# Kernel optimization log

Hardware: AMD Instinct MI355X
Metric: run time of the kernel (lower is better)

Reference implementation:

```python
import jax, jax.numpy as jnp
import numpy as np
from jax import lax

N = 100000          # nodes in the AST
D = 128             # embedding_dims
C = 8               # max arity (complete 8-ary tree)
NTYPES = 131        # len(NODE_TYPES)


def setup_inputs() -> dict:
    key = jax.random.key(0)
    k_t, k_e, k_ih, k_hh = jax.random.split(key, 4)

    # --- build complete 8-ary tree structure (numpy, static) ---
    idx = np.arange(1, N)
    par = (idx - 1) // C
    slot = (idx - 1) % C
    children = np.full((N, C), N, dtype=np.int32)   # pad with sentinel N
    children[par, slot] = idx
    num_children = np.bincount(par, minlength=N).astype(np.int32)
    # depth of node i in complete C-ary tree: level d starts at (C^d-1)/(C-1)
    starts = np.array([(C ** d - 1) // (C - 1) for d in range(12)], dtype=np.int64)
    depth = np.searchsorted(starts, np.arange(N), side='right') - 1
    L = int(depth.max()) + 1
    M = int(np.bincount(depth).max())
    level_nodes = np.full((L, M), N, dtype=np.int32)  # deepest level first
    for d in range(L):
        nd = np.nonzero(depth == d)[0].astype(np.int32)
        level_nodes[L - 1 - d, : len(nd)] = nd

    # --- parameters (xavier-ish embedding, small LSTM weights, torch bias init) ---
    emb_table = jax.random.normal(k_e, (NTYPES, D), jnp.float32) * (2.0 / (NTYPES + D)) ** 0.5
    W_ih = jax.random.normal(k_ih, (4 * D, D), jnp.float32) * (2.0 / (5 * D)) ** 0.5
    W_hh = jax.random.normal(k_hh, (4 * D, D), jnp.float32) * (2.0 / (5 * D)) ** 0.5
    b_ih = jnp.zeros((4 * D,), jnp.float32)
    b_hh = jnp.ones((4 * D,), jnp.float32)
    node_types = jax.random.randint(k_t, (N,), 0, NTYPES, dtype=jnp.int32)
    return {
        'emb_table': emb_table, 'W_ih': W_ih, 'W_hh': W_hh,
        'b_ih': b_ih, 'b_hh': b_hh,
        'node_types': node_types,
        'children': jnp.asarray(children),
        'num_children': jnp.asarray(num_children),
        'level_nodes': jnp.asarray(level_nodes),
    }


def _forward(emb_table, W_ih, W_hh, b_ih, b_hh, node_types, children, num_children, level_nodes):
    M = level_nodes.shape[1]
    T = C + 1  # sequence length = parent emb + up to C child results

    def level_step(results, nodes):
        # nodes: [M] node ids for this depth level (sentinel N = padding)
        emb = emb_table[node_types[nodes]]            # [M, D] (OOB gather clips; masked below)
        nc = num_children[nodes]                      # [M]
        cres = results[children[nodes]]               # [M, C, D]; sentinel -> zero row N
        seq = jnp.concatenate([emb[:, None, :], cres], axis=1)  # [M, T, D]

        def cell(carry, xt):
            h, c = carry
            x, t = xt
            gates = x @ W_ih.T + b_ih + h @ W_hh.T + b_hh      # [M, 4D]
            i, f, g, o = jnp.split(gates, 4, axis=-1)
            i = jax.nn.sigmoid(i); f = jax.nn.sigmoid(f)
            g = jnp.tanh(g); o = jax.nn.sigmoid(o)
            c_new = f * c + i * g
            h_new = o * jnp.tanh(c_new)
            valid = (t <= nc)[:, None]                         # steps 0..nc are real
            return (jnp.where(valid, h_new, h), jnp.where(valid, c_new, c)), None

        h0 = jnp.zeros((M, emb_table.shape[1]), emb_table.dtype)
        (h, _), _ = lax.scan(cell, (h0, h0), (seq.transpose(1, 0, 2), jnp.arange(T)))
        out = jnp.where((nc == 0)[:, None], emb, h)   # leaves: raw embedding, no LSTM
        results = results.at[nodes].set(out)
        results = results.at[N].set(0.0)              # keep sentinel row zero
        return results, None

    results0 = jnp.zeros((N + 1, emb_table.shape[1]), emb_table.dtype)
    results, _ = lax.scan(level_step, results0, level_nodes)  # deepest -> root
    return results[0]  # root (Module node) encoding, shape [D]


def reference(emb_table, W_ih, W_hh, b_ih, b_hh, node_types, children, num_children, level_nodes):
    return _forward(emb_table, W_ih, W_hh, b_ih, b_hh,
                    node_types, children, num_children, level_nodes)
```

## Files before the change

### kernel.cpp

```cpp
#include <hip/hip_runtime.h>


#define D 128
#define NTOT 100000
#define NINT 12500

typedef _Float16 f16x8 __attribute__((ext_vector_type(8)));
typedef _Float16 f16x4 __attribute__((ext_vector_type(4)));
typedef float f32x4 __attribute__((ext_vector_type(4)));

__device__ __forceinline__ float fsig(float x) {
    float e = __expf(fminf(-x, 30.f));
    return __builtin_amdgcn_rcpf(1.f + e);
}
__device__ __forceinline__ float ftanh(float x) {
    float e = __expf(fminf(2.f * x, 30.f));
    return (e - 1.f) * __builtin_amdgcn_rcpf(e + 1.f);
}

__global__ void prep_wfrag(const float* __restrict__ W_ih, const float* __restrict__ W_hh,
                           const float* __restrict__ b_ih, const float* __restrict__ b_hh,
                           _Float16* __restrict__ wfrag, float4* __restrict__ bias4)
{
    int t = blockIdx.x * blockDim.x + threadIdx.x;
    if (t < 8 * 4 * 8 * 64) {
        int l  = t & 63;
        int kk = (t >> 6) & 7;
        int ct = (t >> 9) & 3;
        int w  = (t >> 11) & 7;
        int k0 = kk * 32 + ((l >> 4) * 8);
        int c  = ct * 128 + w * 16 + (l & 15);
        const float* src = (k0 < 128) ? (W_ih + (size_t)c * D + k0)
                                      : (W_hh + (size_t)c * D + (k0 - 128));
        f16x8 v;
#pragma unroll
        for (int j = 0; j < 8; ++j) v[j] = (_Float16)src[j];
        *(f16x8*)(wfrag + (size_t)t * 8) = v;
    }
    if (t < D) {
        bias4[t] = make_float4(b_ih[t      ] + b_hh[t      ],
                               b_ih[t + 128] + b_hh[t + 128],
                               b_ih[t + 256] + b_hh[t + 256],
                               b_ih[t + 384] + b_hh[t + 384]);
    }
}

template<int RT>
__global__ __launch_bounds__(512, 2) void lstm_level(
    int start, int count,
    const float* __restrict__ emb, const int* __restrict__ node_types,
    const int* __restrict__ children,
    const _Float16* __restrict__ wfrag, const float4* __restrict__ bias4,
    _Float16* __restrict__ resultsH, float* __restrict__ out)
{
    constexpr int NR  = 16 * RT;
    constexpr int TPR = 512 / NR;
    constexpr int DPT = 128 / TPR;

    __shared__ _Float16 Xh[NR][264];
    __shared__ int chid_s[NR][8];
    __shared__ int chty_s[NR][8];
    __shared__ int ntype_s[NR];

    const int t = threadIdx.x;
    const int w = t >> 6;
    const int l = t & 63;
    const int n0 = start + (int)blockIdx.x * NR;
    const int B  = min(NR, start + count - n0);

    f16x8 bf[4][8];
#pragma unroll
    for (int ct = 0; ct < 4; ++ct)
#pragma unroll
        for (int kk = 0; kk < 8; ++kk)
            bf[ct][kk] = *(const f16x8*)(wfrag + ((size_t)(((w * 4 + ct) * 8 + kk) * 64 + l)) * 8);

    const int dcol = w * 16 + (l & 15);
    const float4 bb = bias4[dcol];

    if (t < NR * 8) {
        int row = t >> 3, slot = t & 7;
        int ch = children[(size_t)(n0 + row) * 8 + slot];
        chid_s[row][slot] = ch;
        chty_s[row][slot] = (ch >= NINT && ch < NTOT) ? node_types[ch] : 0;
    }
    if (t < NR) ntype_s[t] = node_types[n0 + t];
    {
        int row = t / TPR, di = (t % TPR) * DPT;
        if (RT == 2) *(f16x8*)&Xh[row][128 + di] = (f16x8)(_Float16)0.f;
        else         *(f16x4*)&Xh[row][128 + di] = (f16x4)(_Float16)0.f;
    }

    float cr[RT][4], hr[RT][4];
#pragma unroll
    for (int rt = 0; rt < RT; ++rt)
#pragma unroll
        for (int r = 0; r < 4; ++r) { cr[rt][r] = 0.f; hr[rt][r] = 0.f; }

    __syncthreads();

    for (int s = 0; s < 9; ++s) {
        {
            const int row = t / TPR;
            const int di  = (t % TPR) * DPT;
            const float*     srcF = nullptr;
            const _Float16*  srcH = nullptr;
            if (s == 0) {
                srcF = emb + (size_t)ntype_s[row] * D;
            } else {
                int ch = chid_s[row][s - 1];
                if (ch < NINT)      srcH = resultsH + (size_t)ch * D;
                else if (ch < NTOT) srcF = emb + (size_t)chty_s[row][s - 1] * D;
            }
            if (RT == 2) {
                f16x8 v = (f16x8)(_Float16)0.f;
                if (srcH) v = *(const f16x8*)(srcH + di);
                else if (srcF) {
                    float4 a = *(const float4*)(srcF + di);
                    float4 b = *(const float4*)(srcF + di + 4);
                    v[0]=(_Float16)a.x; v[1]=(_Float16)a.y; v[2]=(_Float16)a.z; v[3]=(_Float16)a.w;
                    v[4]=(_Float16)b.x; v[5]=(_Float16)b.y; v[6]=(_Float16)b.z; v[7]=(_Float16)b.w;
                }
                *(f16x8*)&Xh[row][di] = v;
            } else {
                f16x4 v = (f16x4)(_Float16)0.f;
                if (srcH) v = *(const f16x4*)(srcH + di);
                else if (srcF) {
                    float4 a = *(const float4*)(srcF + di);
                    v[0]=(_Float16)a.x; v[1]=(_Float16)a.y; v[2]=(_Float16)a.z; v[3]=(_Float16)a.w;
                }
                *(f16x4*)&Xh[row][di] = v;
            }
        }
        __syncthreads();

        f32x4 acc[RT][4];
#pragma unroll
        for (int rt = 0; rt < RT; ++rt)
#pragma unroll
            for (int ct = 0; ct < 4; ++ct) acc[rt][ct] = (f32x4){0.f, 0.f, 0.f, 0.f};
#pragma unroll
        for (int kk = 0; kk < 8; ++kk) {
#pragma unroll
            for (int rt = 0; rt < RT; ++rt) {
                f16x8 a = *(const f16x8*)&Xh[rt * 16 + (l & 15)][kk * 32 + ((l >> 4) * 8)];
#pragma unroll
                for (int ct = 0; ct < 4; ++ct)
                    acc[rt][ct] = __builtin_amdgcn_mfma_f32_16x16x32_f16(a, bf[ct][kk], acc[rt][ct], 0, 0, 0);
            }
        }
        __syncthreads();

#pragma unroll
        for (int rt = 0; rt < RT; ++rt) {
#pragma unroll
            for (int r = 0; r < 4; ++r) {
                const int row = rt * 16 + ((l >> 4) * 4) + r;
                const bool upd = !(s == 8 && (n0 + row) == NINT - 1);
                if (upd) {
                    float iv = fsig (acc[rt][0][r] + bb.x);
                    float fv = fsig (acc[rt][1][r] + bb.y);
                    float gv = ftanh(acc[rt][2][r] + bb.z);
                    float ov = fsig (acc[rt][3][r] + bb.w);
                    float cn = fv * cr[rt][r] + iv * gv;
                    cr[rt][r] = cn;
                    hr[rt][r] = ov * ftanh(cn);
                }
                if (s < 8) Xh[row][128 + dcol] = (_Float16)hr[rt][r];
            }
        }
    }

#pragma unroll
    for (int rt = 0; rt < RT; ++rt) {
#pragma unroll
        for (int r = 0; r < 4; ++r) {
            const int row = rt * 16 + ((l >> 4) * 4) + r;
            if (row < B) {
                const int node = n0 + row;
                resultsH[(size_t)node * D + dcol] = (_Float16)hr[rt][r];
                if (node == 0) out[dcol] = hr[rt][r];
            }
        }
    }
}

extern "C" void kernel_launch(void* const* d_in, const int* in_sizes, int n_in,
                              void* d_out, int out_size, void* d_ws, size_t ws_size,
                              hipStream_t stream)
{
    const float* emb        = (const float*)d_in[0];
    const float* W_ih       = (const float*)d_in[1];
    const float* W_hh       = (const float*)d_in[2];
    const float* b_ih       = (const float*)d_in[3];
    const float* b_hh       = (const float*)d_in[4];
    const int*   node_types = (const int*)d_in[5];
    const int*   children   = (const int*)d_in[6];

    float* out = (float*)d_out;

    char*      ws       = (char*)d_ws;
    _Float16*  resultsH = (_Float16*)ws;
    size_t     res_b    = (size_t)NINT * D * sizeof(_Float16);
    res_b = (res_b + 255) & ~(size_t)255;
    _Float16*  wfrag    = (_Float16*)(ws + res_b);
    float4*    bias4    = (float4*)(ws + res_b + 262144);

    prep_wfrag<<<64, 256, 0, stream>>>(W_ih, W_hh, b_ih, b_hh, wfrag, bias4);

    lstm_level<2><<<245, 512, 0, stream>>>(4681, 7819, emb, node_types, children,
                                           wfrag, bias4, resultsH, out);
    lstm_level<1><<<256, 512, 0, stream>>>(585, 4096, emb, node_types, children,
                                           wfrag, bias4, resultsH, out);
    lstm_level<1><<<32, 512, 0, stream>>>(73, 512, emb, node_types, children,
                                          wfrag, bias4, resultsH, out);
    lstm_level<1><<<4, 512, 0, stream>>>(9, 64, emb, node_types, children,
                                         wfrag, bias4, resultsH, out);
    lstm_level<1><<<1, 512, 0, stream>>>(1, 8, emb, node_types, children,
                                         wfrag, bias4, resultsH, out);
    lstm_level<1><<<1, 512, 0, stream>>>(0, 1, emb, node_types, children,
                                         wfrag, bias4, resultsH, out);
}
```

Before: 123.3 us.

## Double-buffer LSTM step inputs, fuse weight prep and root level into kernels

Removes the separate weight-fragment prep kernel: each block now loads the fp32 W_ih/W_hh rows and converts them to fp16 MFMA fragments itself. The per-step child gather is software-pipelined two steps ahead into registers, with the LDS input tile double-buffered, cutting one barrier per step. The root level is fused into the last launch through an LDS stash, so one kernel launch goes away. Padding validity now comes from a per-row child bitmask, and the clamps in sigmoid/tanh are dropped. The cost is redundant weight loading in every block and higher register pressure.

New measurement: 225.3 us. +82.8%, slower.

```diff
diff --git a/kernel.cpp b/kernel.cpp
--- a/kernel.cpp
+++ b/kernel.cpp
@@ -7,89 +7,117 @@
 
 typedef _Float16 f16x8 __attribute__((ext_vector_type(8)));
 typedef _Float16 f16x4 __attribute__((ext_vector_type(4)));
-typedef float f32x4 __attribute__((ext_vector_type(4)));
+typedef float    f32x4 __attribute__((ext_vector_type(4)));
 
 __device__ __forceinline__ float fsig(float x) {
-    float e = __expf(fminf(-x, 30.f));
-    return __builtin_amdgcn_rcpf(1.f + e);
+    return __builtin_amdgcn_rcpf(1.f + __expf(-x));
 }
 __device__ __forceinline__ float ftanh(float x) {
-    float e = __expf(fminf(2.f * x, 30.f));
-    return (e - 1.f) * __builtin_amdgcn_rcpf(e + 1.f);
-}
-
-__global__ void prep_wfrag(const float* __restrict__ W_ih, const float* __restrict__ W_hh,
-                           const float* __restrict__ b_ih, const float* __restrict__ b_hh,
-                           _Float16* __restrict__ wfrag, float4* __restrict__ bias4)
-{
-    int t = blockIdx.x * blockDim.x + threadIdx.x;
-    if (t < 8 * 4 * 8 * 64) {
-        int l  = t & 63;
-        int kk = (t >> 6) & 7;
-        int ct = (t >> 9) & 3;
-        int w  = (t >> 11) & 7;
-        int k0 = kk * 32 + ((l >> 4) * 8);
-        int c  = ct * 128 + w * 16 + (l & 15);
-        const float* src = (k0 < 128) ? (W_ih + (size_t)c * D + k0)
-                                      : (W_hh + (size_t)c * D + (k0 - 128));
-        f16x8 v;
-#pragma unroll
-        for (int j = 0; j < 8; ++j) v[j] = (_Float16)src[j];
-        *(f16x8*)(wfrag + (size_t)t * 8) = v;
-    }
-    if (t < D) {
-        bias4[t] = make_float4(b_ih[t      ] + b_hh[t      ],
-                               b_ih[t + 128] + b_hh[t + 128],
-                               b_ih[t + 256] + b_hh[t + 256],
-                               b_ih[t + 384] + b_hh[t + 384]);
-    }
-}
-
-template<int RT>
+    return 1.f - 2.f * __builtin_amdgcn_rcpf(__expf(2.f * x) + 1.f);
+}
+
+template<int DPT> struct XVT;
+template<> struct XVT<8> { using T = f16x8; };
+template<> struct XVT<4> { using T = f16x4; };
+
+template<int RT, bool FUSE_ROOT>
 __global__ __launch_bounds__(512, 2) void lstm_level(
     int start, int count,
     const float* __restrict__ emb, const int* __restrict__ node_types,
     const int* __restrict__ children,
-    const _Float16* __restrict__ wfrag, const float4* __restrict__ bias4,
+    const float* __restrict__ W_ih, const float* __restrict__ W_hh,
+    const float* __restrict__ b_ih, const float* __restrict__ b_hh,
     _Float16* __restrict__ resultsH, float* __restrict__ out)
 {
     constexpr int NR  = 16 * RT;
     constexpr int TPR = 512 / NR;
     constexpr int DPT = 128 / TPR;
-
-    __shared__ _Float16 Xh[NR][264];
-    __shared__ int chid_s[NR][8];
-    __shared__ int chty_s[NR][8];
-    __shared__ int ntype_s[NR];
-
-    const int t = threadIdx.x;
-    const int w = t >> 6;
-    const int l = t & 63;
+    using xvec = typename XVT<DPT>::T;
+
+    __shared__ __align__(16) _Float16 Xh[2][NR][264];
+    __shared__ int      chid_s[NR][8];
+    __shared__ __align__(16) _Float16 Hstash[8][128];
+
+    const int t  = threadIdx.x;
+    const int w  = t >> 6;
+    const int l  = t & 63;
     const int n0 = start + (int)blockIdx.x * NR;
     const int B  = min(NR, start + count - n0);
 
+    const int row = t / TPR;
+    const int di  = (t % TPR) * DPT;
+    const int dcol = w * 16 + (l & 15);
+
+    if (t < NR * 8) {
+        int rr = t >> 3, slot = t & 7;
+        chid_s[rr][slot] = children[(size_t)(n0 + rr) * 8 + slot];
+    }
+    __syncthreads();
+
     f16x8 bf[4][8];
 #pragma unroll
-    for (int ct = 0; ct < 4; ++ct)
-#pragma unroll
-        for (int kk = 0; kk < 8; ++kk)
-            bf[ct][kk] = *(const f16x8*)(wfrag + ((size_t)(((w * 4 + ct) * 8 + kk) * 64 + l)) * 8);
-
-    const int dcol = w * 16 + (l & 15);
-    const float4 bb = bias4[dcol];
-
-    if (t < NR * 8) {
-        int row = t >> 3, slot = t & 7;
-        int ch = children[(size_t)(n0 + row) * 8 + slot];
-        chid_s[row][slot] = ch;
-        chty_s[row][slot] = (ch >= NINT && ch < NTOT) ? node_types[ch] : 0;
-    }
-    if (t < NR) ntype_s[t] = node_types[n0 + t];
-    {
-        int row = t / TPR, di = (t % TPR) * DPT;
-        if (RT == 2) *(f16x8*)&Xh[row][128 + di] = (f16x8)(_Float16)0.f;
-        else         *(f16x4*)&Xh[row][128 + di] = (f16x4)(_Float16)0.f;
-    }
+    for (int ct = 0; ct < 4; ++ct) {
+        const int c = ct * 128 + dcol;
+#pragma unroll
+        for (int kk = 0; kk < 8; ++kk) {
+            const int k0 = (kk & 3) * 32 + ((l >> 4) * 8);
+            const float* src = (kk < 4) ? (W_ih + (size_t)c * D + k0)
+                                        : (W_hh + (size_t)c * D + k0);
+            float4 a = *(const float4*)(src);
+            float4 b = *(const float4*)(src + 4);
+            f16x8 v;
+            v[0]=(_Float16)a.x; v[1]=(_Float16)a.y; v[2]=(_Float16)a.z; v[3]=(_Float16)a.w;
+            v[4]=(_Float16)b.x; v[5]=(_Float16)b.y; v[6]=(_Float16)b.z; v[7]=(_Float16)b.w;
+            bf[ct][kk] = v;
+        }
+    }
+    float4 bb;
+    bb.x = b_ih[dcol      ] + b_hh[dcol      ];
+    bb.y = b_ih[dcol + 128] + b_hh[dcol + 128];
+    bb.z = b_ih[dcol + 256] + b_hh[dcol + 256];
+    bb.w = b_ih[dcol + 384] + b_hh[dcol + 384];
+
+    unsigned amask[RT][4];
+#pragma unroll
+    for (int rt = 0; rt < RT; ++rt)
+#pragma unroll
+        for (int r = 0; r < 4; ++r) {
+            const int r2 = rt * 16 + ((l >> 4) * 4) + r;
+            unsigned m = 1u;
+#pragma unroll
+            for (int slot = 0; slot < 8; ++slot)
+                m |= (chid_s[r2][slot] < NTOT ? 1u : 0u) << (slot + 1);
+            amask[rt][r] = m;
+        }
+
+    auto issue_gather = [&](int s) -> xvec {
+        xvec v = (xvec)(_Float16)0.f;
+        const float*    srcF = nullptr;
+        const _Float16* srcH = nullptr;
+        if (s == 0) {
+            srcF = emb + (size_t)node_types[n0 + row] * D + di;
+        } else {
+            int ch = chid_s[row][s - 1];
+            if (ch < NINT)      srcH = resultsH + (size_t)ch * D + di;
+            else if (ch < NTOT) srcF = emb + (size_t)node_types[ch] * D + di;
+        }
+        if (srcH) {
+            v = *(const xvec*)srcH;
+        } else if (srcF) {
+#pragma unroll
+            for (int q = 0; q < DPT; q += 4) {
+                float4 a = *(const float4*)(srcF + q);
+                v[q+0]=(_Float16)a.x; v[q+1]=(_Float16)a.y;
+                v[q+2]=(_Float16)a.z; v[q+3]=(_Float16)a.w;
+            }
+        }
+        return v;
+    };
+
+    *(xvec*)&Xh[0][row][di]       = issue_gather(0);
+    *(xvec*)&Xh[0][row][128 + di] = (xvec)(_Float16)0.f;
+    xvec xA = issue_gather(1);
+    xvec xB = issue_gather(2);
 
     float cr[RT][4], hr[RT][4];
 #pragma unroll
@@ -97,44 +125,8 @@
 #pragma unroll
         for (int r = 0; r < 4; ++r) { cr[rt][r] = 0.f; hr[rt][r] = 0.f; }
 
-    __syncthreads();
-
-    for (int s = 0; s < 9; ++s) {
-        {
-            const int row = t / TPR;
-            const int di  = (t % TPR) * DPT;
-            const float*     srcF = nullptr;
-            const _Float16*  srcH = nullptr;
-            if (s == 0) {
-                srcF = emb + (size_t)ntype_s[row] * D;
-            } else {
-                int ch = chid_s[row][s - 1];
-                if (ch < NINT)      srcH = resultsH + (size_t)ch * D;
-                else if (ch < NTOT) srcF = emb + (size_t)chty_s[row][s - 1] * D;
-            }
-            if (RT == 2) {
-                f16x8 v = (f16x8)(_Float16)0.f;
-                if (srcH) v = *(const f16x8*)(srcH + di);
-                else if (srcF) {
-                    float4 a = *(const float4*)(srcF + di);
-                    float4 b = *(const float4*)(srcF + di + 4);
-                    v[0]=(_Float16)a.x; v[1]=(_Float16)a.y; v[2]=(_Float16)a.z; v[3]=(_Float16)a.w;
-                    v[4]=(_Float16)b.x; v[5]=(_Float16)b.y; v[6]=(_Float16)b.z; v[7]=(_Float16)b.w;
-                }
-                *(f16x8*)&Xh[row][di] = v;
-            } else {
-                f16x4 v = (f16x4)(_Float16)0.f;
-                if (srcH) v = *(const f16x4*)(srcH + di);
-                else if (srcF) {
-                    float4 a = *(const float4*)(srcF + di);
-                    v[0]=(_Float16)a.x; v[1]=(_Float16)a.y; v[2]=(_Float16)a.z; v[3]=(_Float16)a.w;
-                }
-                *(f16x4*)&Xh[row][di] = v;
-            }
-        }
-        __syncthreads();
-
-        f32x4 acc[RT][4];
+    f32x4 acc[RT][4];
+    auto mfma_phase = [&](int b) {
 #pragma unroll
         for (int rt = 0; rt < RT; ++rt)
 #pragma unroll
@@ -143,20 +135,20 @@
         for (int kk = 0; kk < 8; ++kk) {
 #pragma unroll
             for (int rt = 0; rt < RT; ++rt) {
-                f16x8 a = *(const f16x8*)&Xh[rt * 16 + (l & 15)][kk * 32 + ((l >> 4) * 8)];
+                f16x8 a = *(const f16x8*)&Xh[b][rt * 16 + (l & 15)][kk * 32 + ((l >> 4) * 8)];
 #pragma unroll
                 for (int ct = 0; ct < 4; ++ct)
                     acc[rt][ct] = __builtin_amdgcn_mfma_f32_16x16x32_f16(a, bf[ct][kk], acc[rt][ct], 0, 0, 0);
             }
         }
-        __syncthreads();
-
-#pragma unroll
-        for (int rt = 0; rt < RT; ++rt) {
+    };
+    auto cell_phase = [&](int s, int b, bool always) {
+#pragma unroll
+        for (int rt = 0; rt < RT; ++rt)
 #pragma unroll
             for (int r = 0; r < 4; ++r) {
-                const int row = rt * 16 + ((l >> 4) * 4) + r;
-                const bool upd = !(s == 8 && (n0 + row) == NINT - 1);
+                const int r2 = rt * 16 + ((l >> 4) * 4) + r;
+                const bool upd = always || ((amask[rt][r] >> s) & 1u);
                 if (upd) {
                     float iv = fsig (acc[rt][0][r] + bb.x);
                     float fv = fsig (acc[rt][1][r] + bb.y);
@@ -166,22 +158,66 @@
                     cr[rt][r] = cn;
                     hr[rt][r] = ov * ftanh(cn);
                 }
-                if (s < 8) Xh[row][128 + dcol] = (_Float16)hr[rt][r];
-            }
-        }
-    }
-
-#pragma unroll
-    for (int rt = 0; rt < RT; ++rt) {
+                if (s < 8) Xh[b ^ 1][r2][128 + dcol] = (_Float16)hr[rt][r];
+            }
+    };
+
+    __syncthreads();
+
+    for (int s = 0; s < 9; ++s) {
+        const int b = s & 1;
+        mfma_phase(b);
+        if (s < 8) {
+            *(xvec*)&Xh[b ^ 1][row][di] = xA;
+            xA = xB;
+            if (s <= 5) xB = issue_gather(s + 3);
+        }
+        cell_phase(s, b, false);
+        __syncthreads();
+    }
+
+#pragma unroll
+    for (int rt = 0; rt < RT; ++rt)
 #pragma unroll
         for (int r = 0; r < 4; ++r) {
-            const int row = rt * 16 + ((l >> 4) * 4) + r;
-            if (row < B) {
-                const int node = n0 + row;
-                resultsH[(size_t)node * D + dcol] = (_Float16)hr[rt][r];
-                if (node == 0) out[dcol] = hr[rt][r];
-            }
-        }
+            const int r2 = rt * 16 + ((l >> 4) * 4) + r;
+            if (r2 < B) {
+                resultsH[(size_t)(n0 + r2) * D + dcol] = (_Float16)hr[rt][r];
+                if (FUSE_ROOT && r2 < 8) Hstash[r2][dcol] = (_Float16)hr[rt][r];
+            }
+        }
+
+    if constexpr (FUSE_ROOT) {
+        __syncthreads();
+        {
+            const int nt0 = node_types[0];
+            xvec v0;
+#pragma unroll
+            for (int q = 0; q < DPT; q += 4) {
+                float4 a = *(const float4*)(emb + (size_t)nt0 * D + di + q);
+                v0[q+0]=(_Float16)a.x; v0[q+1]=(_Float16)a.y;
+                v0[q+2]=(_Float16)a.z; v0[q+3]=(_Float16)a.w;
+            }
+            *(xvec*)&Xh[0][row][di]       = v0;
+            *(xvec*)&Xh[0][row][128 + di] = (xvec)(_Float16)0.f;
+        }
+#pragma unroll
+        for (int rt = 0; rt < RT; ++rt)
+#pragma unroll
+            for (int r = 0; r < 4; ++r) { cr[rt][r] = 0.f; hr[rt][r] = 0.f; }
+        __syncthreads();
+
+        for (int s = 0; s < 9; ++s) {
+            const int b = s & 1;
+            mfma_phase(b);
+            if (s < 8) {
+                xvec v = *(const xvec*)&Hstash[s][di];
+                *(xvec*)&Xh[b ^ 1][row][di] = v;
+            }
+            cell_phase(s, b, true);
+            __syncthreads();
+        }
+        if ((l >> 4) == 0) out[dcol] = hr[0][0];
     }
 }
 
@@ -197,27 +233,17 @@
     const int*   node_types = (const int*)d_in[5];
     const int*   children   = (const int*)d_in[6];
 
-    float* out = (float*)d_out;
-
-    char*      ws       = (char*)d_ws;
-    _Float16*  resultsH = (_Float16*)ws;
-    size_t     res_b    = (size_t)NINT * D * sizeof(_Float16);
-    res_b = (res_b + 255) & ~(size_t)255;
-    _Float16*  wfrag    = (_Float16*)(ws + res_b);
-    float4*    bias4    = (float4*)(ws + res_b + 262144);
-
-    prep_wfrag<<<64, 256, 0, stream>>>(W_ih, W_hh, b_ih, b_hh, wfrag, bias4);
-
-    lstm_level<2><<<245, 512, 0, stream>>>(4681, 7819, emb, node_types, children,
-                                           wfrag, bias4, resultsH, out);
-    lstm_level<1><<<256, 512, 0, stream>>>(585, 4096, emb, node_types, children,
-                                           wfrag, bias4, resultsH, out);
-    lstm_level<1><<<32, 512, 0, stream>>>(73, 512, emb, node_types, children,
-                                          wfrag, bias4, resultsH, out);
-    lstm_level<1><<<4, 512, 0, stream>>>(9, 64, emb, node_types, children,
-                                         wfrag, bias4, resultsH, out);
-    lstm_level<1><<<1, 512, 0, stream>>>(1, 8, emb, node_types, children,
-                                         wfrag, bias4, resultsH, out);
-    lstm_level<1><<<1, 512, 0, stream>>>(0, 1, emb, node_types, children,
-                                         wfrag, bias4, resultsH, out);
-}
+    float*    out      = (float*)d_out;
+    _Float16* resultsH = (_Float16*)d_ws;
+
+    lstm_level<2,false><<<245, 512, 0, stream>>>(4681, 7819, emb, node_types, children,
+                                                 W_ih, W_hh, b_ih, b_hh, resultsH, out);
+    lstm_level<1,false><<<256, 512, 0, stream>>>(585, 4096, emb, node_types, children,
+                                                 W_ih, W_hh, b_ih, b_hh, resultsH, out);
+    lstm_level<1,false><<<32, 512, 0, stream>>>(73, 512, emb, node_types, children,
+                                                W_ih, W_hh, b_ih, b_hh, resultsH, out);
+    lstm_level<1,false><<<4, 512, 0, stream>>>(9, 64, emb, node_types, children,
+                                               W_ih, W_hh, b_ih, b_hh, resultsH, out);
+    lstm_level<1,true><<<1, 512, 0, stream>>>(1, 8, emb, node_types, children,
+                                              W_ih, W_hh, b_ih, b_hh, resultsH, out);
+}
```
